# Kernel optimization log

Measured on AMD Instinct MI355X. Metric: run time of the kernel, lower is better.

Reference implementation:

```python
import jax, jax.numpy as jnp
import numpy as np

B, S, H, NH = 2, 2048, 2048, 16
HD = H // NH


def setup_inputs() -> dict:
    key = jax.random.key(0)
    ks = jax.random.split(key, 9)
    s = 1.0 / np.sqrt(H)
    return {
        "hidden_state": jax.random.normal(ks[0], (B, S, H), dtype=jnp.float32),
        "Wq": jax.random.normal(ks[1], (H, H), dtype=jnp.float32) * s,
        "bq": jnp.zeros((H,), dtype=jnp.float32),
        "Wk": jax.random.normal(ks[2], (H, H), dtype=jnp.float32) * s,
        "bk": jnp.zeros((H,), dtype=jnp.float32),
        "Wv": jax.random.normal(ks[3], (H, H), dtype=jnp.float32) * s,
        "bv": jnp.zeros((H,), dtype=jnp.float32),
        "Wo": jax.random.normal(ks[4], (H, H), dtype=jnp.float32) * s,
        "bo": jnp.zeros((H,), dtype=jnp.float32),
    }


def _split_heads(x):
    # [B,S,H] -> [B,NH,S,HD]
    b, s, _ = x.shape
    return x.reshape(b, s, NH, HD).transpose(0, 2, 1, 3)


def reference(hidden_state, Wq, bq, Wk, bk, Wv, bv, Wo, bo):
    q = _split_heads(hidden_state @ Wq.T + bq)
    k = _split_heads(hidden_state @ Wk.T + bk)
    v = _split_heads(hidden_state @ Wv.T + bv)
    scale = 1.0 / jnp.sqrt(jnp.array(HD, dtype=q.dtype))
    scores = jnp.einsum("bhqd,bhkd->bhqk", q, k) * scale
    attn = jax.nn.softmax(scores, axis=-1)
    out = jnp.einsum("bhqk,bhkd->bhqd", attn, v)  # [B,NH,S,HD]
    out = out.transpose(0, 2, 1, 3).reshape(hidden_state.shape[0], -1, H)
    return out @ Wo.T + bo
```

## Files before the change

### kernel.cpp

```cpp
#include <hip/hip_runtime.h>
#include <hip/hip_bf16.h>
#include <stdint.h>

#define B_ 2
#define S_ 2048
#define H_ 2048
#define NH_ 16
#define HD_ 128
#define M_ (B_*S_)

typedef __attribute__((ext_vector_type(8))) short short8_t;
typedef __attribute__((ext_vector_type(4))) float floatx4;
typedef __attribute__((ext_vector_type(16))) float floatx16;

__device__ __forceinline__ short f2bf(float f) {
  union { float f; uint32_t u; } x; x.f = f;
  const uint32_t u = x.u;
  return (short)((u + 0x7FFFu + ((u >> 16) & 1u)) >> 16);
}

__device__ __forceinline__ void gload_lds16(const void* g, void* l) {
  __builtin_amdgcn_global_load_lds(
      (const __attribute__((address_space(1))) void*)g,
      (__attribute__((address_space(3))) void*)l, 16, 0, 0);
}

__global__ __launch_bounds__(256)
void cast_all(const float* __restrict__ h,  const float* __restrict__ wq,
              const float* __restrict__ wk, const float* __restrict__ wv,
              const float* __restrict__ wo,
              short* __restrict__ hB,  short* __restrict__ wqB,
              short* __restrict__ wkB, short* __restrict__ wvB,
              short* __restrict__ woB) {
  const int blk = blockIdx.x;
  const float* src; short* dst; int off;
  if      (blk <  4096) { src = h;  dst = hB;  off = blk; }
  else if (blk <  6144) { src = wq; dst = wqB; off = blk - 4096; }
  else if (blk <  8192) { src = wk; dst = wkB; off = blk - 6144; }
  else if (blk < 10240) { src = wv; dst = wvB; off = blk - 8192; }
  else                  { src = wo; dst = woB; off = blk - 10240; }
  const int i = (off * 256 + threadIdx.x) * 8;
  typedef __attribute__((ext_vector_type(4))) float f4;
  const f4 a = *(const f4*)(src + i);
  const f4 b = *(const f4*)(src + i + 4);
  short8_t o;
  o[0] = f2bf(a[0]); o[1] = f2bf(a[1]); o[2] = f2bf(a[2]); o[3] = f2bf(a[3]);
  o[4] = f2bf(b[0]); o[5] = f2bf(b[1]); o[6] = f2bf(b[2]); o[7] = f2bf(b[3]);
  *(short8_t*)(dst + i) = o;
}

template<int MODE>
__device__ __forceinline__
void gemm_body256(const short* __restrict__ A, const short* __restrict__ Bm,
                  const float* __restrict__ bias, void* __restrict__ C,
                  const int m0, const int n0, const int N, const int K) {
  extern __shared__ short lds[];
  short* As = lds;
  short* Bs = lds + 32768;

  const int tid = threadIdx.x;
  const int w  = tid >> 6, ln = tid & 63;
  const int lr = ln >> 4,  lc = ln & 15;
  const int wm = (w >> 1) << 6;
  const int wn = (w & 1) << 6;

  const int srr = ln >> 2;
  const int sgc = (ln & 3) ^ ((ln >> 3) & 3);

  const short* aSrc0 = A  + (size_t)(m0 + (w * 2 + 0) * 16 + srr) * K + sgc * 8;
  const short* aSrc1 = A  + (size_t)(m0 + (w * 2 + 1) * 16 + srr) * K + sgc * 8;
  const short* bSrc  = Bm + (size_t)(n0 +  w * 16          + srr) * K + sgc * 8;

  const int aDst0 = (w * 2 + 0) * 512;
  const int aDst1 = (w * 2 + 1) * 512;
  const int bDst  =  w * 512;

#define STAGE_(t_) do {                                      \
    const int bq_ = (t_) & 3; const int ko_ = (t_) * 32;     \
    gload_lds16(aSrc0 + ko_, &As[bq_ * 8192 + aDst0]);       \
    gload_lds16(aSrc1 + ko_, &As[bq_ * 8192 + aDst1]);       \
    gload_lds16(bSrc  + ko_, &Bs[bq_ * 4096 + bDst]);        \
  } while (0)

  STAGE_(0); STAGE_(1); STAGE_(2);

  floatx4 acc[4][4] = {};
  const int swz = (lr ^ ((lc >> 1) & 3)) << 3;
  const int aro = (wm + lc) * 32 + swz;
  const int bro = (wn + lc) * 32 + swz;

  asm volatile("s_waitcnt vmcnt(6)" ::: "memory");
  __builtin_amdgcn_s_barrier();

  const int NT = K >> 5;
  for (int t = 0; t < NT; ++t) {
    const int cb = t & 3;
    short8_t af[4], bf[4];
#pragma unroll
    for (int i = 0; i < 4; ++i)
      af[i] = *(const short8_t*)&As[cb * 8192 + aro + i * 512];
#pragma unroll
    for (int j = 0; j < 4; ++j)
      bf[j] = *(const short8_t*)&Bs[cb * 4096 + bro + j * 512];

    if (t + 3 < NT) STAGE_(t + 3);

    __builtin_amdgcn_s_barrier();
    asm volatile("s_waitcnt lgkmcnt(0)" ::: "memory");
    __builtin_amdgcn_sched_barrier(0);
    __builtin_amdgcn_s_setprio(1);
#pragma unroll
    for (int i = 0; i < 4; ++i)
#pragma unroll
      for (int j = 0; j < 4; ++j)
        acc[i][j] = __builtin_amdgcn_mfma_f32_16x16x32_bf16(af[i], bf[j], acc[i][j], 0, 0, 0);
    __builtin_amdgcn_s_setprio(0);
    __builtin_amdgcn_sched_barrier(0);
    if (t < NT - 3)       asm volatile("s_waitcnt vmcnt(6)" ::: "memory");
    else if (t == NT - 3) asm volatile("s_waitcnt vmcnt(3)" ::: "memory");
    else if (t == NT - 2) asm volatile("s_waitcnt vmcnt(0)" ::: "memory");
    __builtin_amdgcn_s_barrier();
  }
#undef STAGE_

#pragma unroll
  for (int i = 0; i < 4; ++i) {
#pragma unroll
    for (int j = 0; j < 4; ++j) {
      const int col = n0 + wn + j * 16 + lc;
      const float bv = bias[col];
#pragma unroll
      for (int r = 0; r < 4; ++r) {
        const int row = m0 + wm + i * 16 + lr * 4 + r;
        const float v = acc[i][j][r] + bv;
        if (MODE == 1) ((float*)C)[(size_t)row * N + col] = v;
        else           ((short*)C)[(size_t)row * N + col] = f2bf(v);
      }
    }
  }
}

__global__ __launch_bounds__(512, 2)
void gemm_qkv(const short* __restrict__ A,
              const short* __restrict__ W0, const short* __restrict__ W1, const short* __restrict__ W2,
              const float* __restrict__ b0, const float* __restrict__ b1, const float* __restrict__ b2,
              short* __restrict__ C0, short* __restrict__ C1, short* __restrict__ C2) {
  const int sel = blockIdx.x >> 4;
  const short* Bm   = sel == 0 ? W0 : (sel == 1 ? W1 : W2);
  const float* bias = sel == 0 ? b0 : (sel == 1 ? b1 : b2);
  short* C          = sel == 0 ? C0 : (sel == 1 ? C1 : C2);
  gemm_body256<0>(A, Bm, bias, C, blockIdx.y * 256, (blockIdx.x & 15) * 128, H_, H_);
}

__global__ __launch_bounds__(512, 2)
void gemm_out(const short* __restrict__ A, const short* __restrict__ Bm,
              const float* __restrict__ bias, float* __restrict__ C) {
  gemm_body256<1>(A, Bm, bias, C, blockIdx.y * 256, blockIdx.x * 128, H_, H_);
}

__global__ __launch_bounds__(256)
void arrange_v(const short* __restrict__ V, short* __restrict__ Vt) {
  __shared__ short T[64][72];
  const int b = blockIdx.z;
  const int s0 = blockIdx.x * 64, c0 = blockIdx.y * 64;
  const int t = threadIdx.x;
  const int r = t >> 3, c8 = (t & 7) * 8;
  const int kt = s0 >> 6;
#pragma unroll
  for (int p = 0; p < 2; ++p) {
    const int row = p * 32 + r;
    *(short8_t*)&T[row][c8] =
        *(const short8_t*)&V[(size_t)(b * S_ + s0 + row) * H_ + c0 + c8];
  }
  __syncthreads();
#pragma unroll
  for (int p = 0; p < 2; ++p) {
    const int row = p * 32 + r;
    const int gcol = c0 + row;
    const int hh = gcol >> 7, d = gcol & 127;
    short8_t o;
#pragma unroll
    for (int j = 0; j < 8; ++j) o[j] = T[c8 + j][row];
    const int chunk = (c8 >> 3) ^ (d & 7);
    *(short8_t*)&Vt[((((size_t)(b * 16 + hh) * 32 + kt) * 128 + d) << 6) + chunk * 8] = o;
  }
}

__global__ __launch_bounds__(256, 2)
void attention(const short* __restrict__ Q, const short* __restrict__ Kg,
               const short* __restrict__ Vt, short* __restrict__ O) {
  __shared__ short Ks[2][64 * 128];
  __shared__ short Vs[2][128 * 64];
  __shared__ float invLds[128];

  const int tid = threadIdx.x;
  const int wv = tid >> 6, ln = tid & 63;
  const int l32 = ln & 31, lh = ln >> 5;
  const int bh = blockIdx.y, b = bh >> 4, h = bh & 15;
  const int qw = blockIdx.x * 128 + wv * 32;

  const short* Qp  = Q  + ((size_t)(b * S_ + qw)) * H_ + h * HD_;
  const short* VtB = Vt + (size_t)bh * (S_ * HD_) + (size_t)wv * 2048 + ln * 8;

  const short* kp[4];
#pragma unroll
  for (int j = 0; j < 4; ++j) {
    const int key = wv * 16 + j * 4 + (ln >> 4);
    const int sc = (ln & 15) ^ (key & 7);
    kp[j] = Kg + (size_t)(b * S_ + key) * H_ + h * HD_ + sc * 8;
  }

  short8_t qf[8];
#pragma unroll
  for (int ksq = 0; ksq < 8; ++ksq)
    qf[ksq] = *(const short8_t*)&Qp[(size_t)l32 * H_ + ksq * 16 + lh * 8];

  floatx16 oacc[4] = {};
  float lsum = 0.f;
  const float csc = 0.08838834764831845f * 1.4426950408889634f;

#pragma unroll
  for (int j = 0; j < 4; ++j)
    gload_lds16(kp[j], &Ks[0][(wv * 16 + j * 4) * 128]);
#pragma unroll
  for (int j = 0; j < 4; ++j)
    gload_lds16(VtB + j * 512, &Vs[0][wv * 2048 + j * 512]);

  for (int kt = 0; kt < S_ / 64; ++kt) {
    const int cur = kt & 1;
    __syncthreads();

    if (kt + 1 < S_ / 64) {
      const size_t kadv = (size_t)(kt + 1) * 64 * H_;
#pragma unroll
      for (int j = 0; j < 4; ++j)
        gload_lds16(kp[j] + kadv, &Ks[cur ^ 1][(wv * 16 + j * 4) * 128]);
#pragma unroll
      for (int j = 0; j < 4; ++j)
        gload_lds16(VtB + (size_t)(kt + 1) * 8192 + j * 512, &Vs[cur ^ 1][wv * 2048 + j * 512]);
    }

    floatx16 sacc[2] = {};
#pragma unroll
    for (int kh = 0; kh < 2; ++kh) {
      const int key = kh * 32 + l32;
      const int swk = (key & 7) * 8;
#pragma unroll
      for (int ksq = 0; ksq < 8; ++ksq) {
        const short8_t kf =
            *(const short8_t*)&Ks[cur][key * 128 + (((ksq * 2 + lh) * 8) ^ swk)];
        sacc[kh] = __builtin_amdgcn_mfma_f32_32x32x16_bf16(kf, qf[ksq], sacc[kh], 0, 0, 0);
      }
    }

    int pfr[4][4];
#pragma unroll
    for (int kh = 0; kh < 2; ++kh) {
      uint32_t P[8];
#pragma unroll
      for (int i = 0; i < 8; ++i) {
        const uint32_t u0 = __float_as_uint(exp2f(sacc[kh][2 * i] * csc));
        const uint32_t u1 = __float_as_uint(exp2f(sacc[kh][2 * i + 1] * csc));
        lsum += __uint_as_float(u0 & 0xffff0000u) + __uint_as_float(u1 & 0xffff0000u);
        P[i] = (u0 >> 16) | (u1 & 0xffff0000u);
      }
#pragma unroll
      for (int t = 0; t < 2; ++t)
#pragma unroll
        for (int j = 0; j < 2; ++j) {
          const int a = (int)P[t * 4 + j], bb = (int)P[t * 4 + j + 2];
          const int as = __shfl_xor(a, 32), bs = __shfl_xor(bb, 32);
          pfr[kh * 2 + t][j]     = lh ? bs : a;
          pfr[kh * 2 + t][j + 2] = lh ? bb : as;
        }
    }

#pragma unroll
    for (int kf = 0; kf < 4; ++kf) {
      union { int i[4]; short8_t s; } pu;
#pragma unroll
      for (int j = 0; j < 4; ++j) pu.i[j] = pfr[kf][j];
#pragma unroll
      for (int dt = 0; dt < 4; ++dt) {
        const int d = dt * 32 + l32;
        const short8_t vf =
            *(const short8_t*)&Vs[cur][d * 64 + (((kf * 2 + lh) * 8) ^ ((d & 7) * 8))];
        oacc[dt] = __builtin_amdgcn_mfma_f32_32x32x16_bf16(pu.s, vf, oacc[dt], 0, 0, 0);
      }
    }
  }

  const float l = lsum + __shfl_xor(lsum, 32);
  invLds[wv * 32 + l32] = 1.0f / l;
  float inv[16];
#pragma unroll
  for (int r = 0; r < 16; ++r)
    inv[r] = invLds[wv * 32 + (r & 3) + 8 * (r >> 2) + 4 * lh];
  short* Op = O + ((size_t)(b * S_ + qw)) * H_ + h * HD_;
#pragma unroll
  for (int dt = 0; dt < 4; ++dt)
#pragma unroll
    for (int r = 0; r < 16; ++r) {
      const int rowl = (r & 3) + 8 * (r >> 2) + 4 * lh;
      Op[(size_t)rowl * H_ + dt * 32 + l32] = f2bf(oacc[dt][r] * inv[r]);
    }
}

extern "C" void kernel_launch(void* const* d_in, const int* in_sizes, int n_in,
                              void* d_out, int out_size, void* d_ws, size_t ws_size,
                              hipStream_t stream) {
  const float* hidden = (const float*)d_in[0];
  const float* Wq = (const float*)d_in[1];
  const float* bq = (const float*)d_in[2];
  const float* Wk = (const float*)d_in[3];
  const float* bk = (const float*)d_in[4];
  const float* Wv = (const float*)d_in[5];
  const float* bv = (const float*)d_in[6];
  const float* Wo = (const float*)d_in[7];
  const float* bo = (const float*)d_in[8];
  float* out = (float*)d_out;

  char* ws = (char*)d_ws;
  short* hB  = (short*)(ws);
  short* WqB = (short*)(ws + (16u << 20));
  short* WkB = (short*)(ws + (24u << 20));
  short* WvB = (short*)(ws + (32u << 20));
  short* WoB = (short*)(ws + (40u << 20));
  short* Qb  = (short*)(ws + (48u << 20));
  short* Kb  = (short*)(ws + (64u << 20));
  short* Vb  = (short*)(ws + (80u << 20));
  short* Vtb = (short*)(ws + (96u << 20));
  short* Ob  = (short*)(ws + (112u << 20));

  constexpr int GEMM_LDS = (4 * 8192 + 4 * 4096) * 2;
  static int lds_set = 0;
  if (!lds_set) {
    lds_set = 1;
    (void)hipFuncSetAttribute((const void*)gemm_qkv,
        hipFuncAttributeMaxDynamicSharedMemorySize, GEMM_LDS);
    (void)hipFuncSetAttribute((const void*)gemm_out,
        hipFuncAttributeMaxDynamicSharedMemorySize, GEMM_LDS);
  }

  cast_all<<<12288, 256, 0, stream>>>(hidden, Wq, Wk, Wv, Wo, hB, WqB, WkB, WvB, WoB);

  gemm_qkv<<<dim3(48, 16), 512, GEMM_LDS, stream>>>(hB, WqB, WkB, WvB, bq, bk, bv, Qb, Kb, Vb);

  arrange_v<<<dim3(S_ / 64, H_ / 64, B_), 256, 0, stream>>>(Vb, Vtb);

  attention<<<dim3(S_ / 128, B_ * NH_), 256, 0, stream>>>(Qb, Kb, Vtb, Ob);

  gemm_out<<<dim3(16, 16), 512, GEMM_LDS, stream>>>(Ob, WoB, bo, out);
}
```

Baseline: 402.4 us.

## Rewrite QKV GEMM with 256x256 tiles, ping-pong LDS pipeline and block swizzle

```diff
diff --git a/kernel.cpp b/kernel.cpp
--- a/kernel.cpp
+++ b/kernel.cpp
@@ -49,6 +49,165 @@
   *(short8_t*)(dst + i) = o;
 }
 
+__device__ __forceinline__
+void gemm256(const short* __restrict__ A, const short* __restrict__ Bm,
+             const float* __restrict__ bias, short* __restrict__ C,
+             const int m0, const int n0, const int N, const int K) {
+  extern __shared__ short lds[];
+  const int tid = threadIdx.x;
+  const int w  = tid >> 6, ln = tid & 63;
+  const int lr = ln >> 4,  lc = ln & 15;
+  const int wm = (w >> 2) << 7;
+  const int wn = (w & 3) << 6;
+
+  const int srow = ln >> 3;
+  const int schk = (ln & 7) ^ srow;
+  const short* aS = A  + (size_t)(m0 + w * 16 + srow) * K + schk * 8;
+  const short* bS = Bm + (size_t)(n0 + w * 16 + srow) * K + schk * 8;
+  const int dA = (w * 16) * 64;
+
+#define SA_LO(u_) do { const int q_ = ((u_) & 1) * 32768;                    \
+    gload_lds16(aS + (u_) * 64,                    &lds[q_ + dA]);           \
+    gload_lds16(aS + (u_) * 64 + (size_t)8 * K,    &lds[q_ + dA + 512]); } while (0)
+#define SA_HI(u_) do { const int q_ = ((u_) & 1) * 32768;                    \
+    gload_lds16(aS + (u_) * 64 + (size_t)128 * K,  &lds[q_ + 8192 + dA]);    \
+    gload_lds16(aS + (u_) * 64 + (size_t)136 * K,  &lds[q_ + 8192 + dA + 512]); } while (0)
+#define SB_LO(u_) do { const int q_ = ((u_) & 1) * 32768;                    \
+    gload_lds16(bS + (u_) * 64,                    &lds[q_ + 16384 + dA]);   \
+    gload_lds16(bS + (u_) * 64 + (size_t)8 * K,    &lds[q_ + 16384 + dA + 512]); } while (0)
+#define SB_HI(u_) do { const int q_ = ((u_) & 1) * 32768;                    \
+    gload_lds16(bS + (u_) * 64 + (size_t)128 * K,  &lds[q_ + 24576 + dA]);   \
+    gload_lds16(bS + (u_) * 64 + (size_t)136 * K,  &lds[q_ + 24576 + dA + 512]); } while (0)
+
+  const int fsw = (lc & 7) << 3;
+  const int k0o = (lr * 8) ^ fsw;
+  const int k1o = (32 + lr * 8) ^ fsw;
+  const int aro = (wm + lc) * 64;
+  const int bro = 16384 + (wn + lc) * 64;
+
+  floatx4 acc[8][4] = {};
+  short8_t af[8], b0f[4], b1f[4];
+
+  const int NT = K >> 6;
+  SA_LO(0); SA_HI(0); SB_LO(0); SB_HI(0);
+  SB_LO(1); SB_HI(1); SA_LO(1);
+  asm volatile("s_waitcnt vmcnt(6)" ::: "memory");
+  __builtin_amdgcn_s_barrier();
+
+  for (int u = 0; u < NT; ++u) {
+    const int Bb = (u & 1) * 32768;
+#pragma unroll
+    for (int mf = 0; mf < 4; ++mf) {
+      af[mf * 2]     = *(const short8_t*)&lds[Bb + aro + mf * 1024 + k0o];
+      af[mf * 2 + 1] = *(const short8_t*)&lds[Bb + aro + mf * 1024 + k1o];
+    }
+#pragma unroll
+    for (int nf = 0; nf < 2; ++nf) {
+      b0f[nf * 2]     = *(const short8_t*)&lds[Bb + bro + nf * 1024 + k0o];
+      b0f[nf * 2 + 1] = *(const short8_t*)&lds[Bb + bro + nf * 1024 + k1o];
+    }
+    if (u + 1 < NT) SA_HI(u + 1);
+    __builtin_amdgcn_s_barrier();
+    asm volatile("s_waitcnt lgkmcnt(0)" ::: "memory");
+    __builtin_amdgcn_sched_barrier(0);
+    __builtin_amdgcn_s_setprio(1);
+#pragma unroll
+    for (int mf = 0; mf < 4; ++mf)
+#pragma unroll
+      for (int nf = 0; nf < 2; ++nf) {
+        acc[mf][nf] = __builtin_amdgcn_mfma_f32_16x16x32_bf16(af[mf*2],   b0f[nf*2],   acc[mf][nf], 0, 0, 0);
+        acc[mf][nf] = __builtin_amdgcn_mfma_f32_16x16x32_bf16(af[mf*2+1], b0f[nf*2+1], acc[mf][nf], 0, 0, 0);
+      }
+    __builtin_amdgcn_s_setprio(0);
+    __builtin_amdgcn_s_barrier();
+#pragma unroll
+    for (int nf = 0; nf < 2; ++nf) {
+      b1f[nf * 2]     = *(const short8_t*)&lds[Bb + bro + (nf + 2) * 1024 + k0o];
+      b1f[nf * 2 + 1] = *(const short8_t*)&lds[Bb + bro + (nf + 2) * 1024 + k1o];
+    }
+    __builtin_amdgcn_s_barrier();
+    asm volatile("s_waitcnt lgkmcnt(0)" ::: "memory");
+    __builtin_amdgcn_sched_barrier(0);
+    __builtin_amdgcn_s_setprio(1);
+#pragma unroll
+    for (int mf = 0; mf < 4; ++mf)
+#pragma unroll
+      for (int nf = 0; nf < 2; ++nf) {
+        acc[mf][nf+2] = __builtin_amdgcn_mfma_f32_16x16x32_bf16(af[mf*2],   b1f[nf*2],   acc[mf][nf+2], 0, 0, 0);
+        acc[mf][nf+2] = __builtin_amdgcn_mfma_f32_16x16x32_bf16(af[mf*2+1], b1f[nf*2+1], acc[mf][nf+2], 0, 0, 0);
+      }
+    __builtin_amdgcn_s_setprio(0);
+    __builtin_amdgcn_s_barrier();
+#pragma unroll
+    for (int mf = 0; mf < 4; ++mf) {
+      af[mf * 2]     = *(const short8_t*)&lds[Bb + aro + 4096 + mf * 1024 + k0o];
+      af[mf * 2 + 1] = *(const short8_t*)&lds[Bb + aro + 4096 + mf * 1024 + k1o];
+    }
+    if (u + 2 < NT) SB_LO(u + 2);
+    __builtin_amdgcn_s_barrier();
+    asm volatile("s_waitcnt lgkmcnt(0)" ::: "memory");
+    __builtin_amdgcn_sched_barrier(0);
+    __builtin_amdgcn_s_setprio(1);
+#pragma unroll
+    for (int mf = 0; mf < 4; ++mf)
+#pragma unroll
+      for (int nf = 0; nf < 2; ++nf) {
+        acc[4+mf][nf+2] = __builtin_amdgcn_mfma_f32_16x16x32_bf16(af[mf*2],   b1f[nf*2],   acc[4+mf][nf+2], 0, 0, 0);
+        acc[4+mf][nf+2] = __builtin_amdgcn_mfma_f32_16x16x32_bf16(af[mf*2+1], b1f[nf*2+1], acc[4+mf][nf+2], 0, 0, 0);
+      }
+    __builtin_amdgcn_s_setprio(0);
+    __builtin_amdgcn_s_barrier();
+    if (u + 2 < NT) { SB_HI(u + 2); SA_LO(u + 2); }
+    __builtin_amdgcn_s_barrier();
+    __builtin_amdgcn_s_setprio(1);
+#pragma unroll
+    for (int mf = 0; mf < 4; ++mf)
+#pragma unroll
+      for (int nf = 0; nf < 2; ++nf) {
+        acc[4+mf][nf] = __builtin_amdgcn_mfma_f32_16x16x32_bf16(af[mf*2],   b0f[nf*2],   acc[4+mf][nf], 0, 0, 0);
+        acc[4+mf][nf] = __builtin_amdgcn_mfma_f32_16x16x32_bf16(af[mf*2+1], b0f[nf*2+1], acc[4+mf][nf], 0, 0, 0);
+      }
+    __builtin_amdgcn_s_setprio(0);
+    if (u + 2 < NT) asm volatile("s_waitcnt vmcnt(6)" ::: "memory");
+    else            asm volatile("s_waitcnt vmcnt(0)" ::: "memory");
+    __builtin_amdgcn_s_barrier();
+  }
+#undef SA_LO
+#undef SA_HI
+#undef SB_LO
+#undef SB_HI
+
+#pragma unroll
+  for (int mf = 0; mf < 8; ++mf) {
+#pragma unroll
+    for (int nf = 0; nf < 4; ++nf) {
+      const int col = n0 + wn + nf * 16 + lc;
+      const float bv = bias[col];
+#pragma unroll
+      for (int r = 0; r < 4; ++r) {
+        const int row = m0 + wm + mf * 16 + lr * 4 + r;
+        C[(size_t)row * N + col] = f2bf(acc[mf][nf][r] + bv);
+      }
+    }
+  }
+}
+
+__global__ __launch_bounds__(512, 2)
+void gemm_qkv(const short* __restrict__ A,
+              const short* __restrict__ W0, const short* __restrict__ W1, const short* __restrict__ W2,
+              const float* __restrict__ b0, const float* __restrict__ b1, const float* __restrict__ b2,
+              short* __restrict__ C0, short* __restrict__ C1, short* __restrict__ C2) {
+  const int f   = blockIdx.y * 24 + blockIdx.x;
+  const int swz = (f & 7) * 48 + (f >> 3);
+  const int mt  = swz / 24;
+  const int xt  = swz - mt * 24;
+  const int sel = xt >> 3, nt = xt & 7;
+  const short* Bm   = sel == 0 ? W0 : (sel == 1 ? W1 : W2);
+  const float* bias = sel == 0 ? b0 : (sel == 1 ? b1 : b2);
+  short* C          = sel == 0 ? C0 : (sel == 1 ? C1 : C2);
+  gemm256(A, Bm, bias, C, mt * 256, nt * 256, H_, H_);
+}
+
 template<int MODE>
 __device__ __forceinline__
 void gemm_body256(const short* __restrict__ A, const short* __restrict__ Bm,
@@ -138,18 +297,6 @@
       }
     }
   }
-}
-
-__global__ __launch_bounds__(512, 2)
-void gemm_qkv(const short* __restrict__ A,
-              const short* __restrict__ W0, const short* __restrict__ W1, const short* __restrict__ W2,
-              const float* __restrict__ b0, const float* __restrict__ b1, const float* __restrict__ b2,
-              short* __restrict__ C0, short* __restrict__ C1, short* __restrict__ C2) {
-  const int sel = blockIdx.x >> 4;
-  const short* Bm   = sel == 0 ? W0 : (sel == 1 ? W1 : W2);
-  const float* bias = sel == 0 ? b0 : (sel == 1 ? b1 : b2);
-  short* C          = sel == 0 ? C0 : (sel == 1 ? C1 : C2);
-  gemm_body256<0>(A, Bm, bias, C, blockIdx.y * 256, (blockIdx.x & 15) * 128, H_, H_);
 }
 
 __global__ __launch_bounds__(512, 2)
@@ -332,23 +479,24 @@
   short* Vtb = (short*)(ws + (96u << 20));
   short* Ob  = (short*)(ws + (112u << 20));
 
-  constexpr int GEMM_LDS = (4 * 8192 + 4 * 4096) * 2;
+  constexpr int QKV_LDS = 2 * 2 * 16384 * 2;
+  constexpr int OUT_LDS = (4 * 8192 + 4 * 4096) * 2;
   static int lds_set = 0;
   if (!lds_set) {
     lds_set = 1;
     (void)hipFuncSetAttribute((const void*)gemm_qkv,
-        hipFuncAttributeMaxDynamicSharedMemorySize, GEMM_LDS);
+        hipFuncAttributeMaxDynamicSharedMemorySize, QKV_LDS);
     (void)hipFuncSetAttribute((const void*)gemm_out,
-        hipFuncAttributeMaxDynamicSharedMemorySize, GEMM_LDS);
+        hipFuncAttributeMaxDynamicSharedMemorySize, OUT_LDS);
   }
 
   cast_all<<<12288, 256, 0, stream>>>(hidden, Wq, Wk, Wv, Wo, hB, WqB, WkB, WvB, WoB);
 
-  gemm_qkv<<<dim3(48, 16), 512, GEMM_LDS, stream>>>(hB, WqB, WkB, WvB, bq, bk, bv, Qb, Kb, Vb);
+  gemm_qkv<<<dim3(24, 16), 512, QKV_LDS, stream>>>(hB, WqB, WkB, WvB, bq, bk, bv, Qb, Kb, Vb);
 
   arrange_v<<<dim3(S_ / 64, H_ / 64, B_), 256, 0, stream>>>(Vb, Vtb);
 
   attention<<<dim3(S_ / 128, B_ * NH_), 256, 0, stream>>>(Qb, Kb, Vtb, Ob);
 
-  gemm_out<<<dim3(16, 16), 512, GEMM_LDS, stream>>>(Ob, WoB, bo, out);
-}
+  gemm_out<<<dim3(16, 16), 512, OUT_LDS, stream>>>(Ob, WoB, bo, out);
+}
```

Result: no change. 410.1 us (+1.9%).

## Use 256x256 tiles with split-phase pipelining and XCD-aware mapping for QKV GEMM

Applied to the files above, without the earlier changes.

```diff
diff --git a/kernel.cpp b/kernel.cpp
--- a/kernel.cpp
+++ b/kernel.cpp
@@ -49,6 +49,127 @@
   *(short8_t*)(dst + i) = o;
 }
 
+__device__ __forceinline__
+void gemm256(const short* __restrict__ A, const short* __restrict__ Bm,
+             const float* __restrict__ bias, short* __restrict__ C,
+             const int m0, const int n0, const int N, const int K) {
+  extern __shared__ short lds[];
+  const int tid = threadIdx.x;
+  const int w  = tid >> 6, ln = tid & 63;
+  const int lr = ln >> 4,  lc = ln & 15;
+  const int wm = (w >> 2) << 7;
+  const int wn = (w & 3) << 6;
+
+  const int srr = ln >> 2;
+  const int sgc = (ln & 3) ^ ((ln >> 3) & 3);
+  const short* aS0 = A  + (size_t)(m0 + w * 32 +      srr) * K + sgc * 8;
+  const short* aS1 = A  + (size_t)(m0 + w * 32 + 16 + srr) * K + sgc * 8;
+  const short* bS0 = Bm + (size_t)(n0 + w * 32 +      srr) * K + sgc * 8;
+  const short* bS1 = Bm + (size_t)(n0 + w * 32 + 16 + srr) * K + sgc * 8;
+  const int dA0 = w * 1024;
+  const int dA1 = w * 1024 + 512;
+
+#define SA_(u_) do { const int s_ = ((u_) & 3) * 16384;            \
+    gload_lds16(aS0 + (size_t)(u_) * 32, &lds[s_ + dA0]);          \
+    gload_lds16(aS1 + (size_t)(u_) * 32, &lds[s_ + dA1]); } while (0)
+#define SB_(u_) do { const int s_ = ((u_) & 3) * 16384 + 8192;     \
+    gload_lds16(bS0 + (size_t)(u_) * 32, &lds[s_ + dA0]);          \
+    gload_lds16(bS1 + (size_t)(u_) * 32, &lds[s_ + dA1]); } while (0)
+
+  const int swz = (lr ^ ((lc >> 1) & 3)) << 3;
+  const int aro = (wm + lc) * 32 + swz;
+  const int bro = 8192 + (wn + lc) * 32 + swz;
+
+  floatx4 acc[8][4] = {};
+  short8_t aLo[4], aHi[4], bf[4];
+
+  const int NT = K >> 5;
+  SA_(0); SB_(0); SA_(1); SB_(1); SA_(2); SB_(2);
+  asm volatile("s_waitcnt vmcnt(8)" ::: "memory");
+  __builtin_amdgcn_s_barrier();
+#pragma unroll
+  for (int mf = 0; mf < 4; ++mf)
+    aLo[mf] = *(const short8_t*)&lds[aro + mf * 512];
+
+  for (int u = 0; u < NT; ++u) {
+    const int sb = (u & 3) * 16384;
+    __builtin_amdgcn_s_barrier();
+    asm volatile("s_waitcnt lgkmcnt(0)" ::: "memory");
+    __builtin_amdgcn_sched_barrier(0);
+#pragma unroll
+    for (int nf = 0; nf < 4; ++nf)
+      bf[nf] = *(const short8_t*)&lds[sb + bro + nf * 512];
+    __builtin_amdgcn_sched_barrier(0);
+#pragma unroll
+    for (int mf = 0; mf < 4; ++mf)
+      aHi[mf] = *(const short8_t*)&lds[sb + aro + 2048 + mf * 512];
+    if (u + 3 < NT) SA_(u + 3);
+    __builtin_amdgcn_sched_barrier(0);
+    asm volatile("s_waitcnt lgkmcnt(4)" ::: "memory");
+    __builtin_amdgcn_sched_barrier(0);
+    __builtin_amdgcn_s_setprio(1);
+#pragma unroll
+    for (int mf = 0; mf < 4; ++mf)
+#pragma unroll
+      for (int nf = 0; nf < 4; ++nf)
+        acc[mf][nf] = __builtin_amdgcn_mfma_f32_16x16x32_bf16(aLo[mf], bf[nf], acc[mf][nf], 0, 0, 0);
+    __builtin_amdgcn_s_setprio(0);
+    __builtin_amdgcn_s_barrier();
+    asm volatile("s_waitcnt lgkmcnt(0)" ::: "memory");
+    if (u < NT - 3) asm volatile("s_waitcnt vmcnt(6)" ::: "memory");
+    else            asm volatile("s_waitcnt vmcnt(0)" ::: "memory");
+    __builtin_amdgcn_sched_barrier(0);
+    {
+      const int un = (u + 1 < NT) ? u + 1 : u;
+      const int sbn = (un & 3) * 16384;
+#pragma unroll
+      for (int mf = 0; mf < 4; ++mf)
+        aLo[mf] = *(const short8_t*)&lds[sbn + aro + mf * 512];
+    }
+    if (u + 3 < NT) SB_(u + 3);
+    __builtin_amdgcn_sched_barrier(0);
+    __builtin_amdgcn_s_setprio(1);
+#pragma unroll
+    for (int mf = 0; mf < 4; ++mf)
+#pragma unroll
+      for (int nf = 0; nf < 4; ++nf)
+        acc[4 + mf][nf] = __builtin_amdgcn_mfma_f32_16x16x32_bf16(aHi[mf], bf[nf], acc[4 + mf][nf], 0, 0, 0);
+    __builtin_amdgcn_s_setprio(0);
+  }
+#undef SA_
+#undef SB_
+
+#pragma unroll
+  for (int mf = 0; mf < 8; ++mf) {
+#pragma unroll
+    for (int nf = 0; nf < 4; ++nf) {
+      const int col = n0 + wn + nf * 16 + lc;
+      const float bv = bias[col];
+#pragma unroll
+      for (int r = 0; r < 4; ++r) {
+        const int row = m0 + wm + mf * 16 + lr * 4 + r;
+        C[(size_t)row * N + col] = f2bf(acc[mf][nf][r] + bv);
+      }
+    }
+  }
+}
+
+__global__ __launch_bounds__(512, 2)
+void gemm_qkv(const short* __restrict__ A,
+              const short* __restrict__ W0, const short* __restrict__ W1, const short* __restrict__ W2,
+              const float* __restrict__ b0, const float* __restrict__ b1, const float* __restrict__ b2,
+              short* __restrict__ C0, short* __restrict__ C1, short* __restrict__ C2) {
+  const int f   = blockIdx.y * 24 + blockIdx.x;
+  const int xcd = f & 7, s = f >> 3;
+  const int xt  = xcd * 3 + (s >> 4);
+  const int mt  = s & 15;
+  const int sel = xt >> 3, nt = xt & 7;
+  const short* Bm   = sel == 0 ? W0 : (sel == 1 ? W1 : W2);
+  const float* bias = sel == 0 ? b0 : (sel == 1 ? b1 : b2);
+  short* C          = sel == 0 ? C0 : (sel == 1 ? C1 : C2);
+  gemm256(A, Bm, bias, C, mt * 256, nt * 256, H_, H_);
+}
+
 template<int MODE>
 __device__ __forceinline__
 void gemm_body256(const short* __restrict__ A, const short* __restrict__ Bm,
@@ -95,13 +216,13 @@
   const int NT = K >> 5;
   for (int t = 0; t < NT; ++t) {
     const int cb = t & 3;
-    short8_t af[4], bf[4];
+    short8_t af[4], bfr[4];
 #pragma unroll
     for (int i = 0; i < 4; ++i)
       af[i] = *(const short8_t*)&As[cb * 8192 + aro + i * 512];
 #pragma unroll
     for (int j = 0; j < 4; ++j)
-      bf[j] = *(const short8_t*)&Bs[cb * 4096 + bro + j * 512];
+      bfr[j] = *(const short8_t*)&Bs[cb * 4096 + bro + j * 512];
 
     if (t + 3 < NT) STAGE_(t + 3);
 
@@ -113,7 +234,7 @@
     for (int i = 0; i < 4; ++i)
 #pragma unroll
       for (int j = 0; j < 4; ++j)
-        acc[i][j] = __builtin_amdgcn_mfma_f32_16x16x32_bf16(af[i], bf[j], acc[i][j], 0, 0, 0);
+        acc[i][j] = __builtin_amdgcn_mfma_f32_16x16x32_bf16(af[i], bfr[j], acc[i][j], 0, 0, 0);
     __builtin_amdgcn_s_setprio(0);
     __builtin_amdgcn_sched_barrier(0);
     if (t < NT - 3)       asm volatile("s_waitcnt vmcnt(6)" ::: "memory");
@@ -138,18 +259,6 @@
       }
     }
   }
-}
-
-__global__ __launch_bounds__(512, 2)
-void gemm_qkv(const short* __restrict__ A,
-              const short* __restrict__ W0, const short* __restrict__ W1, const short* __restrict__ W2,
-              const float* __restrict__ b0, const float* __restrict__ b1, const float* __restrict__ b2,
-              short* __restrict__ C0, short* __restrict__ C1, short* __restrict__ C2) {
-  const int sel = blockIdx.x >> 4;
-  const short* Bm   = sel == 0 ? W0 : (sel == 1 ? W1 : W2);
-  const float* bias = sel == 0 ? b0 : (sel == 1 ? b1 : b2);
-  short* C          = sel == 0 ? C0 : (sel == 1 ? C1 : C2);
-  gemm_body256<0>(A, Bm, bias, C, blockIdx.y * 256, (blockIdx.x & 15) * 128, H_, H_);
 }
 
 __global__ __launch_bounds__(512, 2)
@@ -332,23 +441,24 @@
   short* Vtb = (short*)(ws + (96u << 20));
   short* Ob  = (short*)(ws + (112u << 20));
 
-  constexpr int GEMM_LDS = (4 * 8192 + 4 * 4096) * 2;
+  constexpr int QKV_LDS = 4 * 16384 * 2;
+  constexpr int OUT_LDS = (4 * 8192 + 4 * 4096) * 2;
   static int lds_set = 0;
   if (!lds_set) {
     lds_set = 1;
     (void)hipFuncSetAttribute((const void*)gemm_qkv,
-        hipFuncAttributeMaxDynamicSharedMemorySize, GEMM_LDS);
+        hipFuncAttributeMaxDynamicSharedMemorySize, QKV_LDS);
     (void)hipFuncSetAttribute((const void*)gemm_out,
-        hipFuncAttributeMaxDynamicSharedMemorySize, GEMM_LDS);
+        hipFuncAttributeMaxDynamicSharedMemorySize, OUT_LDS);
   }
 
   cast_all<<<12288, 256, 0, stream>>>(hidden, Wq, Wk, Wv, Wo, hB, WqB, WkB, WvB, WoB);
 
-  gemm_qkv<<<dim3(48, 16), 512, GEMM_LDS, stream>>>(hB, WqB, WkB, WvB, bq, bk, bv, Qb, Kb, Vb);
+  gemm_qkv<<<dim3(24, 16), 512, QKV_LDS, stream>>>(hB, WqB, WkB, WvB, bq, bk, bv, Qb, Kb, Vb);
 
   arrange_v<<<dim3(S_ / 64, H_ / 64, B_), 256, 0, stream>>>(Vb, Vtb);
 
   attention<<<dim3(S_ / 128, B_ * NH_), 256, 0, stream>>>(Qb, Kb, Vtb, Ob);
 
-  gemm_out<<<dim3(16, 16), 512, GEMM_LDS, stream>>>(Ob, WoB, bo, out);
-}
+  gemm_out<<<dim3(16, 16), 512, OUT_LDS, stream>>>(Ob, WoB, bo, out);
+}
```

Measured after the change: 397.6 us. No clear change (-1.2%).
